# Optimization experiments

Hardware: AMD Instinct MI355X
Metric: run time of the kernel (lower is better)

The kernel has to match this reference:

```python
import jax, jax.numpy as jnp
import numpy as np

NUM_NODES = 50000
NUM_EDGES = 800000
NUM_FEATURES = 128
HIDDEN = 128
NUM_CLASSES = 40


def setup_inputs() -> dict:
    key = jax.random.key(0)
    ks = jax.random.split(key, 10)
    x = jax.random.normal(ks[0], (NUM_NODES, NUM_FEATURES), dtype=jnp.float32)
    edge_index = jax.random.randint(ks[1], (2, NUM_EDGES), 0, NUM_NODES, dtype=jnp.int32)
    def glorot(k, fan_in, fan_out):
        s = jnp.sqrt(6.0 / (fan_in + fan_out))
        return jax.random.uniform(k, (fan_in, fan_out), jnp.float32, -s, s)
    return {
        "x": x,
        "edge_index": edge_index,
        "W1": glorot(ks[2], NUM_FEATURES, HIDDEN), "b1": jnp.zeros((HIDDEN,), jnp.float32),
        "W2": glorot(ks[3], HIDDEN, HIDDEN),       "b2": jnp.zeros((HIDDEN,), jnp.float32),
        "W3": glorot(ks[4], HIDDEN, HIDDEN),       "b3": jnp.zeros((HIDDEN,), jnp.float32),
        "Wc": glorot(ks[5], HIDDEN, NUM_CLASSES),  "bc": jnp.zeros((NUM_CLASSES,), jnp.float32),
    }


def _gcn_norm(edge_index, num_nodes, dtype):
    # add self-loops, symmetric normalization D^{-1/2} (A+I) D^{-1/2}
    loops = jnp.arange(num_nodes, dtype=edge_index.dtype)
    src = jnp.concatenate([edge_index[0], loops])
    dst = jnp.concatenate([edge_index[1], loops])
    deg = jax.ops.segment_sum(jnp.ones_like(dst, dtype=dtype), dst, num_segments=num_nodes)
    dinv = jnp.where(deg > 0, jax.lax.rsqrt(deg), 0.0)
    norm = dinv[src] * dinv[dst]  # [E + N]
    return src, dst, norm


def _gcn_conv(h, W, b, src, dst, norm, num_nodes):
    h = h @ W                                  # [N, out]
    msg = h[src] * norm[:, None]               # gather + scale  [E+N, out]
    agg = jax.ops.segment_sum(msg, dst, num_segments=num_nodes)
    return agg + b


def reference(x, edge_index, W1, b1, W2, b2, W3, b3, Wc, bc):
    N = x.shape[0]
    src, dst, norm = _gcn_norm(edge_index, N, x.dtype)
    h = jax.nn.relu(_gcn_conv(x, W1, b1, src, dst, norm, N))
    h = jax.nn.relu(_gcn_conv(h, W2, b2, src, dst, norm, N))
    h = jax.nn.relu(_gcn_conv(h, W3, b3, src, dst, norm, N))
    out = h @ Wc + bc
    return (out, h)
```

## Files before the change

kernel.cpp:

```cpp
#include <hip/hip_runtime.h>

typedef float f32x4 __attribute__((ext_vector_type(4)));
typedef short s16x8 __attribute__((ext_vector_type(8)));

__device__ __forceinline__ float us2f(unsigned short u) {
    union { unsigned int i; float f; } v;
    v.i = ((unsigned int)u) << 16;
    return v.f;
}
__device__ __forceinline__ unsigned short f2us(float f) {
    union { unsigned int i; float f; } v; v.f = f;
    unsigned int r = v.i + 0x7fff + ((v.i >> 16) & 1);
    return (unsigned short)(r >> 16);
}

__global__ void k_wprep(const float* __restrict__ W1, const float* __restrict__ W2,
                        const float* __restrict__ W3, const float* __restrict__ Wc,
                        unsigned short* __restrict__ img, int* __restrict__ bcnt) {
    int b = blockIdx.x >> 7;
    int n = threadIdx.x;
    if (b >= 4) { bcnt[n] = 0; bcnt[n + 128] = 0; return; }
    int k = blockIdx.x & 127;
    unsigned short *H, *L;
    float f;
    if (b < 3) {
        const float* W = (b == 0) ? W1 : ((b == 1) ? W2 : W3);
        H = img + b * 32768; L = H + 16384;
        f = W[k * 128 + n];
    } else {
        if (n >= 48) return;
        H = img + 3 * 32768; L = H + 6144;
        f = (n < 40) ? Wc[k * 40 + n] : 0.f;
    }
    unsigned short h = f2us(f);
    unsigned short l = f2us(f - us2f(h));
    int idx = n * 128 + ((((k >> 3) ^ (n & 15))) << 3) + (k & 7);
    H[idx] = h; L[idx] = l;
}

__global__ __launch_bounds__(256) void k_hist(const int* __restrict__ dst, int E, int chunk,
                                              int* __restrict__ bcnt) {
    __shared__ int cnt[256];
    int t = threadIdx.x;
    cnt[t] = 0; __syncthreads();
    int s = blockIdx.x * chunk;
    int e = s + chunk; if (e > E) e = E;
    for (int i = s + t; i < e; i += 256) atomicAdd(&cnt[dst[i] >> 8], 1);
    __syncthreads();
    if (cnt[t]) atomicAdd(&bcnt[t], cnt[t]);
}

__global__ void k_bscan(const int* __restrict__ bcnt, int* __restrict__ bofs,
                        int* __restrict__ gcur) {
    __shared__ int s[256];
    int t = threadIdx.x;
    int v = bcnt[t];
    s[t] = v; __syncthreads();
    for (int off = 1; off < 256; off <<= 1) {
        int x = (t >= off) ? s[t - off] : 0;
        __syncthreads();
        s[t] += x;
        __syncthreads();
    }
    int ex = s[t] - v;
    bofs[t] = ex; gcur[t] = ex;
    if (t == 255) bofs[256] = s[255];
}

__global__ __launch_bounds__(256) void k_scatter1(const int* __restrict__ src,
                                                  const int* __restrict__ dst, int E, int chunk,
                                                  int* __restrict__ gcur,
                                                  unsigned int* __restrict__ pk) {
    __shared__ int cnt[256];
    int t = threadIdx.x;
    cnt[t] = 0; __syncthreads();
    int s = blockIdx.x * chunk;
    int e = s + chunk; if (e > E) e = E;
    for (int i = s + t; i < e; i += 256) atomicAdd(&cnt[dst[i] >> 8], 1);
    __syncthreads();
    int base = atomicAdd(&gcur[t], cnt[t]);
    cnt[t] = base;
    __syncthreads();
    for (int i = s + t; i < e; i += 256) {
        int d = dst[i];
        int slot = atomicAdd(&cnt[d >> 8], 1);
        pk[slot] = ((unsigned int)src[i] << 8) | (unsigned int)(d & 255);
    }
}

__global__ __launch_bounds__(256) void k_degscan(const unsigned int* __restrict__ pk,
                                                 const int* __restrict__ bofs,
                                                 int* __restrict__ row_ptr,
                                                 int* __restrict__ bsum,
                                                 float* __restrict__ dinv, int N) {
    __shared__ int cnt[256];
    __shared__ int s[256];
    int t = threadIdx.x, b = blockIdx.x;
    cnt[t] = 0; __syncthreads();
    int s0 = bofs[b], s1 = bofs[b + 1];
    for (int i = s0 + t; i < s1; i += 256) atomicAdd(&cnt[pk[i] & 255], 1);
    __syncthreads();
    int v = cnt[t];
    s[t] = v; __syncthreads();
    for (int off = 1; off < 256; off <<= 1) {
        int x = (t >= off) ? s[t - off] : 0;
        __syncthreads();
        s[t] += x;
        __syncthreads();
    }
    int node = (b << 8) + t;
    if (node < N) {
        row_ptr[node] = s[t] - v;
        dinv[node] = rsqrtf((float)(v + 1));
    }
    if (t == 255) bsum[b] = s[255];
}

__global__ void k_scan2(int* __restrict__ bsum, int nb) {
    __shared__ int s[256];
    int t = threadIdx.x;
    int v = (t < nb) ? bsum[t] : 0;
    s[t] = v; __syncthreads();
    for (int off = 1; off < 256; off <<= 1) {
        int x = (t >= off) ? s[t - off] : 0;
        __syncthreads();
        s[t] += x;
        __syncthreads();
    }
    if (t < nb) bsum[t] = s[t] - v;
}

__global__ __launch_bounds__(256) void k_scatter2(const unsigned int* __restrict__ pk,
                                                  const int* __restrict__ bofs,
                                                  int* __restrict__ row_ptr,
                                                  const int* __restrict__ bsum,
                                                  int* __restrict__ csr, int N, int E) {
    __shared__ int cur[256];
    int t = threadIdx.x, b = blockIdx.x;
    int node = (b << 8) + t;
    int rp = 0;
    if (node < N) {
        rp = row_ptr[node] + bsum[b];
        row_ptr[node] = rp;
    }
    cur[t] = rp;
    __syncthreads();
    int s = bofs[b], e = bofs[b + 1];
    for (int i = s + t; i < e; i += 256) {
        unsigned int v = pk[i];
        int slot = atomicAdd(&cur[v & 255], 1);
        csr[slot] = (int)(v >> 8);
    }
    if (node == N - 1) row_ptr[N] = E;
}

template <bool ABF16>
__global__ __launch_bounds__(256) void k_gemm128m(const void* __restrict__ Ap,
                                                  const unsigned short* __restrict__ img,
                                                  const float* __restrict__ dinv,
                                                  unsigned short* __restrict__ M, int N) {
    __shared__ __align__(16) unsigned short WsH[16384];
    __shared__ __align__(16) unsigned short WsL[16384];
    int t = threadIdx.x;
    {
        const uint4* s = (const uint4*)img;
        uint4* dH = (uint4*)WsH; uint4* dL = (uint4*)WsL;
#pragma unroll
        for (int i = 0; i < 8; i++) dH[t + i * 256] = s[t + i * 256];
#pragma unroll
        for (int i = 0; i < 8; i++) dL[t + i * 256] = s[2048 + t + i * 256];
    }
    __syncthreads();

    int w = t >> 6, lane = t & 63;
    int m = lane & 15, q = lane >> 4;
    int row0 = blockIdx.x * 64 + w * 16;
    int gr = row0 + m;
    int grc = (gr < N) ? gr : (N - 1);
    const float* A32 = (const float*)Ap + (size_t)grc * 128;
    const unsigned short* A16 = (const unsigned short*)Ap + (size_t)grc * 128;
    int nbase = m * 128;

    f32x4 acc[8];
#pragma unroll
    for (int cb = 0; cb < 8; cb++) { acc[cb][0]=0.f; acc[cb][1]=0.f; acc[cb][2]=0.f; acc[cb][3]=0.f; }

#pragma unroll
    for (int ks = 0; ks < 4; ks++) {
        union { unsigned short u[8]; s16x8 v; } ah, al;
        if constexpr (ABF16) {
            ah.v = *(const s16x8*)&A16[ks * 32 + q * 8];
        } else {
            float4 f0 = ((const float4*)A32)[ks * 8 + q * 2];
            float4 f1 = ((const float4*)A32)[ks * 8 + q * 2 + 1];
            float fv[8] = {f0.x, f0.y, f0.z, f0.w, f1.x, f1.y, f1.z, f1.w};
#pragma unroll
            for (int j = 0; j < 8; j++) {
                unsigned short h = f2us(fv[j]);
                ah.u[j] = h;
                al.u[j] = f2us(fv[j] - us2f(h));
            }
        }
        int koff = (((ks * 4 + q) ^ m) & 15) << 3;
#pragma unroll
        for (int cb = 0; cb < 8; cb++) {
            int o = cb * 2048 + nbase + koff;
            s16x8 wh = *(const s16x8*)&WsH[o];
            s16x8 wl = *(const s16x8*)&WsL[o];
            acc[cb] = __builtin_amdgcn_mfma_f32_16x16x32_bf16(ah.v, wh, acc[cb], 0, 0, 0);
            acc[cb] = __builtin_amdgcn_mfma_f32_16x16x32_bf16(ah.v, wl, acc[cb], 0, 0, 0);
            if constexpr (!ABF16)
                acc[cb] = __builtin_amdgcn_mfma_f32_16x16x32_bf16(al.v, wh, acc[cb], 0, 0, 0);
        }
    }

#pragma unroll
    for (int r = 0; r < 4; r++) {
        int grow = row0 + q * 4 + r;
        if (grow < N) {
            float dv = dinv[grow];
#pragma unroll
            for (int cb = 0; cb < 8; cb++)
                M[(size_t)grow * 128 + cb * 16 + m] = f2us(acc[cb][r] * dv);
        }
    }
}

__global__ __launch_bounds__(256) void k_gemm40m(const float* __restrict__ A,
                                                 const unsigned short* __restrict__ img,
                                                 const float* __restrict__ bc,
                                                 float* __restrict__ out, int N) {
    __shared__ __align__(16) unsigned short WsH[6144];
    __shared__ __align__(16) unsigned short WsL[6144];
    int t = threadIdx.x;
    {
        const uint4* s = (const uint4*)img;
        uint4* dH = (uint4*)WsH; uint4* dL = (uint4*)WsL;
#pragma unroll
        for (int i = 0; i < 3; i++) dH[t + i * 256] = s[t + i * 256];
#pragma unroll
        for (int i = 0; i < 3; i++) dL[t + i * 256] = s[768 + t + i * 256];
    }
    __syncthreads();

    int w = t >> 6, lane = t & 63;
    int m = lane & 15, q = lane >> 4;
    int row0 = blockIdx.x * 64 + w * 16;
    int gr = row0 + m;
    int grc = (gr < N) ? gr : (N - 1);
    const float4* Arow = (const float4*)(A + (size_t)grc * 128);
    int nbase = m * 128;

    f32x4 acc[3];
#pragma unroll
    for (int cb = 0; cb < 3; cb++) { acc[cb][0]=0.f; acc[cb][1]=0.f; acc[cb][2]=0.f; acc[cb][3]=0.f; }

#pragma unroll
    for (int ks = 0; ks < 4; ks++) {
        float4 f0 = Arow[ks * 8 + q * 2];
        float4 f1 = Arow[ks * 8 + q * 2 + 1];
        float fv[8] = {f0.x, f0.y, f0.z, f0.w, f1.x, f1.y, f1.z, f1.w};
        union { unsigned short u[8]; s16x8 v; } ah, al;
#pragma unroll
        for (int j = 0; j < 8; j++) {
            unsigned short h = f2us(fv[j]);
            ah.u[j] = h;
            al.u[j] = f2us(fv[j] - us2f(h));
        }
        int koff = (((ks * 4 + q) ^ m) & 15) << 3;
#pragma unroll
        for (int cb = 0; cb < 3; cb++) {
            int o = cb * 2048 + nbase + koff;
            s16x8 wh = *(const s16x8*)&WsH[o];
            s16x8 wl = *(const s16x8*)&WsL[o];
            acc[cb] = __builtin_amdgcn_mfma_f32_16x16x32_bf16(ah.v, wh, acc[cb], 0, 0, 0);
            acc[cb] = __builtin_amdgcn_mfma_f32_16x16x32_bf16(ah.v, wl, acc[cb], 0, 0, 0);
            acc[cb] = __builtin_amdgcn_mfma_f32_16x16x32_bf16(al.v, wh, acc[cb], 0, 0, 0);
        }
    }

#pragma unroll
    for (int r = 0; r < 4; r++) {
        int grow = row0 + q * 4 + r;
        if (grow < N) {
#pragma unroll
            for (int cb = 0; cb < 3; cb++) {
                int col = cb * 16 + m;
                if (col < 40) out[(size_t)grow * 40 + col] = acc[cb][r] + bc[col];
            }
        }
    }
}

template <bool OUT_BF16>
__global__ __launch_bounds__(256) void k_gather(const unsigned short* __restrict__ M,
                                                const int* __restrict__ csr,
                                                const int* __restrict__ row_ptr,
                                                const float* __restrict__ dinv,
                                                const float* __restrict__ bias,
                                                void* __restrict__ H, int N) {
    int w    = (blockIdx.x << 2) + (threadIdx.x >> 6);
    int lane = threadIdx.x & 63;
    if (w >= N) return;
    int g  = lane >> 4;
    int sl = lane & 15;

    const uint4* M16 = (const uint4*)M;
    float acc[8];
#pragma unroll
    for (int i = 0; i < 8; i++) acc[i] = 0.f;

    auto accum = [&](uint4 tv) {
        unsigned int uu[4] = {tv.x, tv.y, tv.z, tv.w};
#pragma unroll
        for (int i = 0; i < 4; i++) {
            acc[2 * i]     += us2f((unsigned short)(uu[i] & 0xffffu));
            acc[2 * i + 1] += us2f((unsigned short)(uu[i] >> 16));
        }
    };

    if (g == 0) accum(M16[(size_t)w * 16 + sl]);

    int s0 = row_ptr[w], s1 = row_ptr[w + 1];
    for (int base = s0; base < s1; base += 64) {
        int n = s1 - base; if (n > 64) n = 64;
        int idx = (lane < n) ? csr[base + lane] : 0;
        int full = n >> 2;
        int rem  = n & 3;
        int j = 0;
        for (; j + 4 <= full; j += 4) {
            int u0 = __shfl(idx, (j + 0) * 4 + g);
            int u1 = __shfl(idx, (j + 1) * 4 + g);
            int u2 = __shfl(idx, (j + 2) * 4 + g);
            int u3 = __shfl(idx, (j + 3) * 4 + g);
            uint4 t0 = M16[(size_t)u0 * 16 + sl];
            uint4 t1 = M16[(size_t)u1 * 16 + sl];
            uint4 t2 = M16[(size_t)u2 * 16 + sl];
            uint4 t3 = M16[(size_t)u3 * 16 + sl];
            accum(t0); accum(t1); accum(t2); accum(t3);
        }
        for (; j < full; j++) {
            int u = __shfl(idx, j * 4 + g);
            accum(M16[(size_t)u * 16 + sl]);
        }
        int ur = __shfl(idx, ((full << 2) + g) & 63);
        if (g < rem) accum(M16[(size_t)ur * 16 + sl]);
    }

#pragma unroll
    for (int i = 0; i < 8; i++) {
        acc[i] += __shfl_xor(acc[i], 16);
        acc[i] += __shfl_xor(acc[i], 32);
    }

    float dv = dinv[w];
    const float4* b4 = (const float4*)bias;
    float4 b0 = b4[sl * 2], b1 = b4[sl * 2 + 1];
    float o[8];
    o[0] = fmaxf(fmaf(dv, acc[0], b0.x), 0.f);
    o[1] = fmaxf(fmaf(dv, acc[1], b0.y), 0.f);
    o[2] = fmaxf(fmaf(dv, acc[2], b0.z), 0.f);
    o[3] = fmaxf(fmaf(dv, acc[3], b0.w), 0.f);
    o[4] = fmaxf(fmaf(dv, acc[4], b1.x), 0.f);
    o[5] = fmaxf(fmaf(dv, acc[5], b1.y), 0.f);
    o[6] = fmaxf(fmaf(dv, acc[6], b1.z), 0.f);
    o[7] = fmaxf(fmaf(dv, acc[7], b1.w), 0.f);

    if (g == 0) {
        if constexpr (OUT_BF16) {
            uint4 p;
            p.x = (unsigned int)f2us(o[0]) | ((unsigned int)f2us(o[1]) << 16);
            p.y = (unsigned int)f2us(o[2]) | ((unsigned int)f2us(o[3]) << 16);
            p.z = (unsigned int)f2us(o[4]) | ((unsigned int)f2us(o[5]) << 16);
            p.w = (unsigned int)f2us(o[6]) | ((unsigned int)f2us(o[7]) << 16);
            ((uint4*)H)[(size_t)w * 16 + sl] = p;
        } else {
            float4* H4 = (float4*)H;
            H4[(size_t)w * 32 + sl * 2]     = make_float4(o[0], o[1], o[2], o[3]);
            H4[(size_t)w * 32 + sl * 2 + 1] = make_float4(o[4], o[5], o[6], o[7]);
        }
    }
}

extern "C" void kernel_launch(void* const* d_in, const int* in_sizes, int n_in,
                              void* d_out, int out_size, void* d_ws, size_t ws_size,
                              hipStream_t stream) {
    const float* x  = (const float*)d_in[0];
    const int*   ei = (const int*)d_in[1];
    const float* W1 = (const float*)d_in[2];
    const float* b1 = (const float*)d_in[3];
    const float* W2 = (const float*)d_in[4];
    const float* b2 = (const float*)d_in[5];
    const float* W3 = (const float*)d_in[6];
    const float* b3 = (const float*)d_in[7];
    const float* Wc = (const float*)d_in[8];
    const float* bc = (const float*)d_in[9];

    const int N = in_sizes[0] / 128;
    const int E = in_sizes[1] / 2;
    const int* src = ei;
    const int* dst = ei + E;

    char* ws = (char*)d_ws;
    size_t off = 0;
    auto alloc = [&](size_t bytes) -> void* {
        void* p = ws + off;
        off = (off + bytes + 255) & ~(size_t)255;
        return p;
    };
    unsigned short* Mbuf = (unsigned short*)alloc((size_t)N * 128 * 2);
    unsigned short* Hb   = (unsigned short*)alloc((size_t)N * 128 * 2);
    unsigned int* pk     = (unsigned int*)alloc((size_t)E * 4);
    unsigned short* img  = (unsigned short*)alloc((3 * 32768 + 2 * 6144) * 2);
    float* dinv    = (float*)alloc((size_t)N * 4);
    int*   row_ptr = (int*)alloc((size_t)(N + 1) * 4);
    int*   csr     = (int*)alloc((size_t)E * 4);
    int*   bcnt    = (int*)alloc(256 * 4);
    int*   bofs    = (int*)alloc(257 * 4);
    int*   gcur    = (int*)alloc(256 * 4);
    int*   bsum    = (int*)alloc(256 * 4);

    float* out  = (float*)d_out;
    float* hbuf = out + (size_t)N * 40;

    const int nb  = (N + 255) / 256;
    const int NB  = (N + 255) >> 8;
    const int G1  = 256;
    const int chunk = (E + G1 - 1) / G1;

    k_wprep<<<513, 128, 0, stream>>>(W1, W2, W3, Wc, img, bcnt);

    k_hist<<<G1, 256, 0, stream>>>(dst, E, chunk, bcnt);
    k_bscan<<<1, 256, 0, stream>>>(bcnt, bofs, gcur);
    k_scatter1<<<G1, 256, 0, stream>>>(src, dst, E, chunk, gcur, pk);
    k_degscan<<<NB, 256, 0, stream>>>(pk, bofs, row_ptr, bsum, dinv, N);
    k_scan2<<<1, 256, 0, stream>>>(bsum, nb);
    k_scatter2<<<NB, 256, 0, stream>>>(pk, bofs, row_ptr, bsum, csr, N, E);

    const int gb  = (N + 63) / 64;
    const int gab = (N + 3) / 4;

    k_gemm128m<false><<<gb, 256, 0, stream>>>(x, img, dinv, Mbuf, N);
    k_gather<true><<<gab, 256, 0, stream>>>(Mbuf, csr, row_ptr, dinv, b1, Hb, N);
    k_gemm128m<true><<<gb, 256, 0, stream>>>(Hb, img + 32768, dinv, Mbuf, N);
    k_gather<true><<<gab, 256, 0, stream>>>(Mbuf, csr, row_ptr, dinv, b2, Hb, N);
    k_gemm128m<true><<<gb, 256, 0, stream>>>(Hb, img + 2 * 32768, dinv, Mbuf, N);
    k_gather<false><<<gab, 256, 0, stream>>>(Mbuf, csr, row_ptr, dinv, b3, hbuf, N);
    k_gemm40m<<<gb, 256, 0, stream>>>(hbuf, img + 3 * 32768, bc, out, N);
}
```

Baseline: 282.8 us.

## Fuse CSR build stages and overlap first GEMM with edge scatter

Merges weight prep with the histogram and uses a last-block-done pattern to do the bucket scan in the same kernel. The first GEMM runs in the same launch as the edge scatter. The degree scan, block-sum scan and CSR scatter become one kernel that uses an atomic counter plus a spin-wait flag as a grid barrier. To let the first GEMM run before degrees are known, the source-side dinv scaling moves from the GEMM epilogue into the gather. This adds a per-neighbor dinv load in every aggregation. The aim is fewer kernel launches and less serialization, but the spin-wait relies on all blocks being co-resident.

After: 288.1 us. No clear change (+1.9%).

```diff
diff --git a/kernel.cpp b/kernel.cpp
--- a/kernel.cpp
+++ b/kernel.cpp
@@ -14,154 +14,68 @@
     return (unsigned short)(r >> 16);
 }
 
-__global__ void k_wprep(const float* __restrict__ W1, const float* __restrict__ W2,
-                        const float* __restrict__ W3, const float* __restrict__ Wc,
-                        unsigned short* __restrict__ img, int* __restrict__ bcnt) {
-    int b = blockIdx.x >> 7;
-    int n = threadIdx.x;
-    if (b >= 4) { bcnt[n] = 0; bcnt[n + 128] = 0; return; }
-    int k = blockIdx.x & 127;
-    unsigned short *H, *L;
-    float f;
-    if (b < 3) {
-        const float* W = (b == 0) ? W1 : ((b == 1) ? W2 : W3);
-        H = img + b * 32768; L = H + 16384;
-        f = W[k * 128 + n];
-    } else {
-        if (n >= 48) return;
-        H = img + 3 * 32768; L = H + 6144;
-        f = (n < 40) ? Wc[k * 40 + n] : 0.f;
-    }
-    unsigned short h = f2us(f);
-    unsigned short l = f2us(f - us2f(h));
-    int idx = n * 128 + ((((k >> 3) ^ (n & 15))) << 3) + (k & 7);
-    H[idx] = h; L[idx] = l;
-}
-
-__global__ __launch_bounds__(256) void k_hist(const int* __restrict__ dst, int E, int chunk,
-                                              int* __restrict__ bcnt) {
+__global__ __launch_bounds__(256) void k_prep_hist(const float* __restrict__ W1,
+                                                   const float* __restrict__ W2,
+                                                   const float* __restrict__ W3,
+                                                   const float* __restrict__ Wc,
+                                                   unsigned short* __restrict__ img,
+                                                   const int* __restrict__ dst, int E, int chunk,
+                                                   int* __restrict__ bcnt, int* __restrict__ done,
+                                                   int* __restrict__ bofs, int* __restrict__ gcur) {
     __shared__ int cnt[256];
+    __shared__ int lastflag;
     int t = threadIdx.x;
+    if (blockIdx.x < 256) {
+        int r = (blockIdx.x << 1) | (t >> 7);
+        int b = r >> 7, k = r & 127, n = t & 127;
+        unsigned short *H, *L;
+        float f;
+        if (b < 3) {
+            const float* W = (b == 0) ? W1 : ((b == 1) ? W2 : W3);
+            H = img + b * 32768; L = H + 16384;
+            f = W[k * 128 + n];
+        } else {
+            if (n >= 48) return;
+            H = img + 3 * 32768; L = H + 6144;
+            f = (n < 40) ? Wc[k * 40 + n] : 0.f;
+        }
+        unsigned short h = f2us(f);
+        unsigned short l = f2us(f - us2f(h));
+        int idx = n * 128 + ((((k >> 3) ^ (n & 15))) << 3) + (k & 7);
+        H[idx] = h; L[idx] = l;
+        return;
+    }
     cnt[t] = 0; __syncthreads();
-    int s = blockIdx.x * chunk;
-    int e = s + chunk; if (e > E) e = E;
-    for (int i = s + t; i < e; i += 256) atomicAdd(&cnt[dst[i] >> 8], 1);
-    __syncthreads();
-    if (cnt[t]) atomicAdd(&bcnt[t], cnt[t]);
-}
-
-__global__ void k_bscan(const int* __restrict__ bcnt, int* __restrict__ bofs,
-                        int* __restrict__ gcur) {
-    __shared__ int s[256];
-    int t = threadIdx.x;
-    int v = bcnt[t];
-    s[t] = v; __syncthreads();
+    int blk = blockIdx.x - 256;
+    int s0 = blk * chunk;
+    int s1 = s0 + chunk; if (s1 > E) s1 = E;
+    for (int i = s0 + t; i < s1; i += 256) atomicAdd(&cnt[dst[i] >> 8], 1);
+    __syncthreads();
+    int c = cnt[t];
+    if (c) atomicAdd(&bcnt[t], c);
+    __syncthreads();
+    if (t == 0) { __threadfence(); lastflag = (atomicAdd(done, 1) == 255); }
+    __syncthreads();
+    if (!lastflag) return;
+    int v = __hip_atomic_load(&bcnt[t], __ATOMIC_RELAXED, __HIP_MEMORY_SCOPE_AGENT);
+    cnt[t] = v; __syncthreads();
     for (int off = 1; off < 256; off <<= 1) {
-        int x = (t >= off) ? s[t - off] : 0;
-        __syncthreads();
-        s[t] += x;
-        __syncthreads();
-    }
-    int ex = s[t] - v;
+        int x = (t >= off) ? cnt[t - off] : 0;
+        __syncthreads();
+        cnt[t] += x;
+        __syncthreads();
+    }
+    int ex = cnt[t] - v;
     bofs[t] = ex; gcur[t] = ex;
-    if (t == 255) bofs[256] = s[255];
-}
-
-__global__ __launch_bounds__(256) void k_scatter1(const int* __restrict__ src,
-                                                  const int* __restrict__ dst, int E, int chunk,
-                                                  int* __restrict__ gcur,
-                                                  unsigned int* __restrict__ pk) {
-    __shared__ int cnt[256];
-    int t = threadIdx.x;
-    cnt[t] = 0; __syncthreads();
-    int s = blockIdx.x * chunk;
-    int e = s + chunk; if (e > E) e = E;
-    for (int i = s + t; i < e; i += 256) atomicAdd(&cnt[dst[i] >> 8], 1);
-    __syncthreads();
-    int base = atomicAdd(&gcur[t], cnt[t]);
-    cnt[t] = base;
-    __syncthreads();
-    for (int i = s + t; i < e; i += 256) {
-        int d = dst[i];
-        int slot = atomicAdd(&cnt[d >> 8], 1);
-        pk[slot] = ((unsigned int)src[i] << 8) | (unsigned int)(d & 255);
-    }
-}
-
-__global__ __launch_bounds__(256) void k_degscan(const unsigned int* __restrict__ pk,
-                                                 const int* __restrict__ bofs,
-                                                 int* __restrict__ row_ptr,
-                                                 int* __restrict__ bsum,
-                                                 float* __restrict__ dinv, int N) {
-    __shared__ int cnt[256];
-    __shared__ int s[256];
-    int t = threadIdx.x, b = blockIdx.x;
-    cnt[t] = 0; __syncthreads();
-    int s0 = bofs[b], s1 = bofs[b + 1];
-    for (int i = s0 + t; i < s1; i += 256) atomicAdd(&cnt[pk[i] & 255], 1);
-    __syncthreads();
-    int v = cnt[t];
-    s[t] = v; __syncthreads();
-    for (int off = 1; off < 256; off <<= 1) {
-        int x = (t >= off) ? s[t - off] : 0;
-        __syncthreads();
-        s[t] += x;
-        __syncthreads();
-    }
-    int node = (b << 8) + t;
-    if (node < N) {
-        row_ptr[node] = s[t] - v;
-        dinv[node] = rsqrtf((float)(v + 1));
-    }
-    if (t == 255) bsum[b] = s[255];
-}
-
-__global__ void k_scan2(int* __restrict__ bsum, int nb) {
-    __shared__ int s[256];
-    int t = threadIdx.x;
-    int v = (t < nb) ? bsum[t] : 0;
-    s[t] = v; __syncthreads();
-    for (int off = 1; off < 256; off <<= 1) {
-        int x = (t >= off) ? s[t - off] : 0;
-        __syncthreads();
-        s[t] += x;
-        __syncthreads();
-    }
-    if (t < nb) bsum[t] = s[t] - v;
-}
-
-__global__ __launch_bounds__(256) void k_scatter2(const unsigned int* __restrict__ pk,
-                                                  const int* __restrict__ bofs,
-                                                  int* __restrict__ row_ptr,
-                                                  const int* __restrict__ bsum,
-                                                  int* __restrict__ csr, int N, int E) {
-    __shared__ int cur[256];
-    int t = threadIdx.x, b = blockIdx.x;
-    int node = (b << 8) + t;
-    int rp = 0;
-    if (node < N) {
-        rp = row_ptr[node] + bsum[b];
-        row_ptr[node] = rp;
-    }
-    cur[t] = rp;
-    __syncthreads();
-    int s = bofs[b], e = bofs[b + 1];
-    for (int i = s + t; i < e; i += 256) {
-        unsigned int v = pk[i];
-        int slot = atomicAdd(&cur[v & 255], 1);
-        csr[slot] = (int)(v >> 8);
-    }
-    if (node == N - 1) row_ptr[N] = E;
+    if (t == 255) bofs[256] = cnt[255];
 }
 
 template <bool ABF16>
-__global__ __launch_bounds__(256) void k_gemm128m(const void* __restrict__ Ap,
-                                                  const unsigned short* __restrict__ img,
-                                                  const float* __restrict__ dinv,
-                                                  unsigned short* __restrict__ M, int N) {
-    __shared__ __align__(16) unsigned short WsH[16384];
-    __shared__ __align__(16) unsigned short WsL[16384];
-    int t = threadIdx.x;
+__device__ __forceinline__ void gemm128_core(const void* __restrict__ Ap,
+                                             const unsigned short* __restrict__ img,
+                                             unsigned short* __restrict__ M, int N,
+                                             int bid, int t,
+                                             unsigned short* WsH, unsigned short* WsL) {
     {
         const uint4* s = (const uint4*)img;
         uint4* dH = (uint4*)WsH; uint4* dL = (uint4*)WsL;
@@ -174,7 +88,7 @@
 
     int w = t >> 6, lane = t & 63;
     int m = lane & 15, q = lane >> 4;
-    int row0 = blockIdx.x * 64 + w * 16;
+    int row0 = bid * 64 + w * 16;
     int gr = row0 + m;
     int grc = (gr < N) ? gr : (N - 1);
     const float* A32 = (const float*)Ap + (size_t)grc * 128;
@@ -218,78 +132,115 @@
     for (int r = 0; r < 4; r++) {
         int grow = row0 + q * 4 + r;
         if (grow < N) {
-            float dv = dinv[grow];
 #pragma unroll
             for (int cb = 0; cb < 8; cb++)
-                M[(size_t)grow * 128 + cb * 16 + m] = f2us(acc[cb][r] * dv);
-        }
-    }
-}
-
-__global__ __launch_bounds__(256) void k_gemm40m(const float* __restrict__ A,
-                                                 const unsigned short* __restrict__ img,
-                                                 const float* __restrict__ bc,
-                                                 float* __restrict__ out, int N) {
-    __shared__ __align__(16) unsigned short WsH[6144];
-    __shared__ __align__(16) unsigned short WsL[6144];
+                M[(size_t)grow * 128 + cb * 16 + m] = f2us(acc[cb][r]);
+        }
+    }
+}
+
+template <bool ABF16>
+__global__ __launch_bounds__(256) void k_gemm128m(const void* __restrict__ Ap,
+                                                  const unsigned short* __restrict__ img,
+                                                  unsigned short* __restrict__ M, int N) {
+    __shared__ __align__(16) unsigned short WsH[16384];
+    __shared__ __align__(16) unsigned short WsL[16384];
+    gemm128_core<ABF16>(Ap, img, M, N, blockIdx.x, threadIdx.x, WsH, WsL);
+}
+
+union KSM {
+    struct { unsigned short H[16384]; unsigned short L[16384]; } w;
+    int cnt[256];
+};
+__global__ __launch_bounds__(256) void k_sc1_gemm1(const int* __restrict__ src,
+                                                   const int* __restrict__ dst, int E, int chunk,
+                                                   int* __restrict__ gcur,
+                                                   unsigned int* __restrict__ pk,
+                                                   const float* __restrict__ x,
+                                                   const unsigned short* __restrict__ img,
+                                                   unsigned short* __restrict__ M, int N) {
+    __shared__ __align__(16) KSM sm;
     int t = threadIdx.x;
-    {
-        const uint4* s = (const uint4*)img;
-        uint4* dH = (uint4*)WsH; uint4* dL = (uint4*)WsL;
-#pragma unroll
-        for (int i = 0; i < 3; i++) dH[t + i * 256] = s[t + i * 256];
-#pragma unroll
-        for (int i = 0; i < 3; i++) dL[t + i * 256] = s[768 + t + i * 256];
-    }
-    __syncthreads();
-
-    int w = t >> 6, lane = t & 63;
-    int m = lane & 15, q = lane >> 4;
-    int row0 = blockIdx.x * 64 + w * 16;
-    int gr = row0 + m;
-    int grc = (gr < N) ? gr : (N - 1);
-    const float4* Arow = (const float4*)(A + (size_t)grc * 128);
-    int nbase = m * 128;
-
-    f32x4 acc[3];
-#pragma unroll
-    for (int cb = 0; cb < 3; cb++) { acc[cb][0]=0.f; acc[cb][1]=0.f; acc[cb][2]=0.f; acc[cb][3]=0.f; }
-
-#pragma unroll
-    for (int ks = 0; ks < 4; ks++) {
-        float4 f0 = Arow[ks * 8 + q * 2];
-        float4 f1 = Arow[ks * 8 + q * 2 + 1];
-        float fv[8] = {f0.x, f0.y, f0.z, f0.w, f1.x, f1.y, f1.z, f1.w};
-        union { unsigned short u[8]; s16x8 v; } ah, al;
-#pragma unroll
-        for (int j = 0; j < 8; j++) {
-            unsigned short h = f2us(fv[j]);
-            ah.u[j] = h;
-            al.u[j] = f2us(fv[j] - us2f(h));
-        }
-        int koff = (((ks * 4 + q) ^ m) & 15) << 3;
-#pragma unroll
-        for (int cb = 0; cb < 3; cb++) {
-            int o = cb * 2048 + nbase + koff;
-            s16x8 wh = *(const s16x8*)&WsH[o];
-            s16x8 wl = *(const s16x8*)&WsL[o];
-            acc[cb] = __builtin_amdgcn_mfma_f32_16x16x32_bf16(ah.v, wh, acc[cb], 0, 0, 0);
-            acc[cb] = __builtin_amdgcn_mfma_f32_16x16x32_bf16(ah.v, wl, acc[cb], 0, 0, 0);
-            acc[cb] = __builtin_amdgcn_mfma_f32_16x16x32_bf16(al.v, wh, acc[cb], 0, 0, 0);
-        }
-    }
-
-#pragma unroll
-    for (int r = 0; r < 4; r++) {
-        int grow = row0 + q * 4 + r;
-        if (grow < N) {
-#pragma unroll
-            for (int cb = 0; cb < 3; cb++) {
-                int col = cb * 16 + m;
-                if (col < 40) out[(size_t)grow * 40 + col] = acc[cb][r] + bc[col];
-            }
-        }
-    }
+    if (blockIdx.x < 256) {
+        sm.cnt[t] = 0; __syncthreads();
+        int s0 = blockIdx.x * chunk;
+        int s1 = s0 + chunk; if (s1 > E) s1 = E;
+        for (int i = s0 + t; i < s1; i += 256) atomicAdd(&sm.cnt[dst[i] >> 8], 1);
+        __syncthreads();
+        int base = atomicAdd(&gcur[t], sm.cnt[t]);
+        sm.cnt[t] = base;
+        __syncthreads();
+        for (int i = s0 + t; i < s1; i += 256) {
+            int d = dst[i];
+            int slot = atomicAdd(&sm.cnt[d >> 8], 1);
+            pk[slot] = ((unsigned int)src[i] << 8) | (unsigned int)(d & 255);
+        }
+        return;
+    }
+    gemm128_core<false>(x, img, M, N, blockIdx.x - 256, t, sm.w.H, sm.w.L);
+}
+
+__global__ __launch_bounds__(256) void k_csr_finish(const unsigned int* __restrict__ pk,
+                                                    const int* __restrict__ bofs,
+                                                    int* __restrict__ row_ptr,
+                                                    int* __restrict__ bsum,
+                                                    float* __restrict__ dinv,
+                                                    int* __restrict__ csr,
+                                                    int N, int E, int nb,
+                                                    int* __restrict__ done2,
+                                                    int* __restrict__ flag3) {
+    __shared__ int cnt[256];
+    __shared__ int s[256];
+    __shared__ int lastflag;
+    int t = threadIdx.x, b = blockIdx.x;
+    cnt[t] = 0; __syncthreads();
+    int s0 = bofs[b], s1 = bofs[b + 1];
+    for (int i = s0 + t; i < s1; i += 256) atomicAdd(&cnt[pk[i] & 255], 1);
+    __syncthreads();
+    int v = cnt[t];
+    s[t] = v; __syncthreads();
+    for (int off = 1; off < 256; off <<= 1) {
+        int x = (t >= off) ? s[t - off] : 0;
+        __syncthreads();
+        s[t] += x;
+        __syncthreads();
+    }
+    int node = (b << 8) + t;
+    int rp_local = s[t] - v;
+    if (node < N) dinv[node] = rsqrtf((float)(v + 1));
+    if (t == 255) __hip_atomic_store(&bsum[b], s[255], __ATOMIC_RELAXED, __HIP_MEMORY_SCOPE_AGENT);
+    __syncthreads();
+    if (t == 0) { __threadfence(); lastflag = (atomicAdd(done2, 1) == nb - 1); }
+    __syncthreads();
+    if (lastflag) {
+        int vv = (t < nb) ? __hip_atomic_load(&bsum[t], __ATOMIC_RELAXED, __HIP_MEMORY_SCOPE_AGENT) : 0;
+        s[t] = vv; __syncthreads();
+        for (int off = 1; off < 256; off <<= 1) {
+            int x = (t >= off) ? s[t - off] : 0;
+            __syncthreads();
+            s[t] += x;
+            __syncthreads();
+        }
+        if (t < nb) __hip_atomic_store(&bsum[t], s[t] - vv, __ATOMIC_RELAXED, __HIP_MEMORY_SCOPE_AGENT);
+        __syncthreads();
+        if (t == 0) { __threadfence(); __hip_atomic_store(flag3, 1, __ATOMIC_RELEASE, __HIP_MEMORY_SCOPE_AGENT); }
+    }
+    if (t == 0) {
+        while (__hip_atomic_load(flag3, __ATOMIC_ACQUIRE, __HIP_MEMORY_SCOPE_AGENT) == 0)
+            __builtin_amdgcn_s_sleep(2);
+    }
+    __syncthreads();
+    int base = __hip_atomic_load(&bsum[b], __ATOMIC_RELAXED, __HIP_MEMORY_SCOPE_AGENT);
+    int rp = 0;
+    if (node < N) { rp = rp_local + base; row_ptr[node] = rp; }
+    cnt[t] = rp;
+    __syncthreads();
+    for (int i = s0 + t; i < s1; i += 256) {
+        unsigned int vpk = pk[i];
+        int slot = atomicAdd(&cnt[vpk & 255], 1);
+        csr[slot] = (int)(vpk >> 8);
+    }
+    if (node == N - 1) row_ptr[N] = E;
 }
 
 template <bool OUT_BF16>
@@ -306,20 +257,21 @@
     int sl = lane & 15;
 
     const uint4* M16 = (const uint4*)M;
+    float dv = dinv[w];
     float acc[8];
 #pragma unroll
     for (int i = 0; i < 8; i++) acc[i] = 0.f;
 
-    auto accum = [&](uint4 tv) {
+    auto accum = [&](uint4 tv, float sc) {
         unsigned int uu[4] = {tv.x, tv.y, tv.z, tv.w};
 #pragma unroll
         for (int i = 0; i < 4; i++) {
-            acc[2 * i]     += us2f((unsigned short)(uu[i] & 0xffffu));
-            acc[2 * i + 1] += us2f((unsigned short)(uu[i] >> 16));
+            acc[2 * i]     = fmaf(sc, us2f((unsigned short)(uu[i] & 0xffffu)), acc[2 * i]);
+            acc[2 * i + 1] = fmaf(sc, us2f((unsigned short)(uu[i] >> 16)), acc[2 * i + 1]);
         }
     };
 
-    if (g == 0) accum(M16[(size_t)w * 16 + sl]);
+    if (g == 0) accum(M16[(size_t)w * 16 + sl], dv);
 
     int s0 = row_ptr[w], s1 = row_ptr[w + 1];
     for (int base = s0; base < s1; base += 64) {
@@ -333,18 +285,19 @@
             int u1 = __shfl(idx, (j + 1) * 4 + g);
             int u2 = __shfl(idx, (j + 2) * 4 + g);
             int u3 = __shfl(idx, (j + 3) * 4 + g);
+            float d0 = dinv[u0], d1 = dinv[u1], d2 = dinv[u2], d3 = dinv[u3];
             uint4 t0 = M16[(size_t)u0 * 16 + sl];
             uint4 t1 = M16[(size_t)u1 * 16 + sl];
             uint4 t2 = M16[(size_t)u2 * 16 + sl];
             uint4 t3 = M16[(size_t)u3 * 16 + sl];
-            accum(t0); accum(t1); accum(t2); accum(t3);
+            accum(t0, d0); accum(t1, d1); accum(t2, d2); accum(t3, d3);
         }
         for (; j < full; j++) {
             int u = __shfl(idx, j * 4 + g);
-            accum(M16[(size_t)u * 16 + sl]);
+            accum(M16[(size_t)u * 16 + sl], dinv[u]);
         }
         int ur = __shfl(idx, ((full << 2) + g) & 63);
-        if (g < rem) accum(M16[(size_t)ur * 16 + sl]);
+        if (g < rem) accum(M16[(size_t)ur * 16 + sl], dinv[ur]);
     }
 
 #pragma unroll
@@ -353,7 +306,6 @@
         acc[i] += __shfl_xor(acc[i], 32);
     }
 
-    float dv = dinv[w];
     const float4* b4 = (const float4*)bias;
     float4 b0 = b4[sl * 2], b1 = b4[sl * 2 + 1];
     float o[8];
@@ -378,6 +330,72 @@
             float4* H4 = (float4*)H;
             H4[(size_t)w * 32 + sl * 2]     = make_float4(o[0], o[1], o[2], o[3]);
             H4[(size_t)w * 32 + sl * 2 + 1] = make_float4(o[4], o[5], o[6], o[7]);
+        }
+    }
+}
+
+__global__ __launch_bounds__(256) void k_gemm40m(const float* __restrict__ A,
+                                                 const unsigned short* __restrict__ img,
+                                                 const float* __restrict__ bc,
+                                                 float* __restrict__ out, int N) {
+    __shared__ __align__(16) unsigned short WsH[6144];
+    __shared__ __align__(16) unsigned short WsL[6144];
+    int t = threadIdx.x;
+    {
+        const uint4* s = (const uint4*)img;
+        uint4* dH = (uint4*)WsH; uint4* dL = (uint4*)WsL;
+#pragma unroll
+        for (int i = 0; i < 3; i++) dH[t + i * 256] = s[t + i * 256];
+#pragma unroll
+        for (int i = 0; i < 3; i++) dL[t + i * 256] = s[768 + t + i * 256];
+    }
+    __syncthreads();
+
+    int w = t >> 6, lane = t & 63;
+    int m = lane & 15, q = lane >> 4;
+    int row0 = blockIdx.x * 64 + w * 16;
+    int gr = row0 + m;
+    int grc = (gr < N) ? gr : (N - 1);
+    const float4* Arow = (const float4*)(A + (size_t)grc * 128);
+    int nbase = m * 128;
+
+    f32x4 acc[3];
+#pragma unroll
+    for (int cb = 0; cb < 3; cb++) { acc[cb][0]=0.f; acc[cb][1]=0.f; acc[cb][2]=0.f; acc[cb][3]=0.f; }
+
+#pragma unroll
+    for (int ks = 0; ks < 4; ks++) {
+        float4 f0 = Arow[ks * 8 + q * 2];
+        float4 f1 = Arow[ks * 8 + q * 2 + 1];
+        float fv[8] = {f0.x, f0.y, f0.z, f0.w, f1.x, f1.y, f1.z, f1.w};
+        union { unsigned short u[8]; s16x8 v; } ah, al;
+#pragma unroll
+        for (int j = 0; j < 8; j++) {
+            unsigned short h = f2us(fv[j]);
+            ah.u[j] = h;
+            al.u[j] = f2us(fv[j] - us2f(h));
+        }
+        int koff = (((ks * 4 + q) ^ m) & 15) << 3;
+#pragma unroll
+        for (int cb = 0; cb < 3; cb++) {
+            int o = cb * 2048 + nbase + koff;
+            s16x8 wh = *(const s16x8*)&WsH[o];
+            s16x8 wl = *(const s16x8*)&WsL[o];
+            acc[cb] = __builtin_amdgcn_mfma_f32_16x16x32_bf16(ah.v, wh, acc[cb], 0, 0, 0);
+            acc[cb] = __builtin_amdgcn_mfma_f32_16x16x32_bf16(ah.v, wl, acc[cb], 0, 0, 0);
+            acc[cb] = __builtin_amdgcn_mfma_f32_16x16x32_bf16(al.v, wh, acc[cb], 0, 0, 0);
+        }
+    }
+
+#pragma unroll
+    for (int r = 0; r < 4; r++) {
+        int grow = row0 + q * 4 + r;
+        if (grow < N) {
+#pragma unroll
+            for (int cb = 0; cb < 3; cb++) {
+                int col = cb * 16 + m;
+                if (col < 40) out[(size_t)grow * 40 + col] = acc[cb][r] + bc[col];
+            }
         }
     }
 }
@@ -415,36 +433,38 @@
     float* dinv    = (float*)alloc((size_t)N * 4);
     int*   row_ptr = (int*)alloc((size_t)(N + 1) * 4);
     int*   csr     = (int*)alloc((size_t)E * 4);
-    int*   bcnt    = (int*)alloc(256 * 4);
+    int*   ctrl    = (int*)alloc(512 * 4);
     int*   bofs    = (int*)alloc(257 * 4);
     int*   gcur    = (int*)alloc(256 * 4);
     int*   bsum    = (int*)alloc(256 * 4);
 
+    int* bcnt  = ctrl;
+    int* done  = ctrl + 256;
+    int* done2 = ctrl + 257;
+    int* flag3 = ctrl + 258;
+
     float* out  = (float*)d_out;
     float* hbuf = out + (size_t)N * 40;
 
     const int nb  = (N + 255) / 256;
-    const int NB  = (N + 255) >> 8;
-    const int G1  = 256;
-    const int chunk = (E + G1 - 1) / G1;
-
-    k_wprep<<<513, 128, 0, stream>>>(W1, W2, W3, Wc, img, bcnt);
-
-    k_hist<<<G1, 256, 0, stream>>>(dst, E, chunk, bcnt);
-    k_bscan<<<1, 256, 0, stream>>>(bcnt, bofs, gcur);
-    k_scatter1<<<G1, 256, 0, stream>>>(src, dst, E, chunk, gcur, pk);
-    k_degscan<<<NB, 256, 0, stream>>>(pk, bofs, row_ptr, bsum, dinv, N);
-    k_scan2<<<1, 256, 0, stream>>>(bsum, nb);
-    k_scatter2<<<NB, 256, 0, stream>>>(pk, bofs, row_ptr, bsum, csr, N, E);
+    const int chunk = (E + 255) / 256;
 
     const int gb  = (N + 63) / 64;
     const int gab = (N + 3) / 4;
 
-    k_gemm128m<false><<<gb, 256, 0, stream>>>(x, img, dinv, Mbuf, N);
+    hipMemsetAsync(ctrl, 0, 512 * 4, stream);
+
+    k_prep_hist<<<512, 256, 0, stream>>>(W1, W2, W3, Wc, img, dst, E, chunk,
+                                         bcnt, done, bofs, gcur);
+    k_sc1_gemm1<<<256 + gb, 256, 0, stream>>>(src, dst, E, chunk, gcur, pk,
+                                              x, img, Mbuf, N);
+    k_csr_finish<<<nb, 256, 0, stream>>>(pk, bofs, row_ptr, bsum, dinv, csr,
+                                         N, E, nb, done2, flag3);
+
     k_gather<true><<<gab, 256, 0, stream>>>(Mbuf, csr, row_ptr, dinv, b1, Hb, N);
-    k_gemm128m<true><<<gb, 256, 0, stream>>>(Hb, img + 32768, dinv, Mbuf, N);
+    k_gemm128m<true><<<gb, 256, 0, stream>>>(Hb, img + 32768, Mbuf, N);
     k_gather<true><<<gab, 256, 0, stream>>>(Mbuf, csr, row_ptr, dinv, b2, Hb, N);
-    k_gemm128m<true><<<gb, 256, 0, stream>>>(Hb, img + 2 * 32768, dinv, Mbuf, N);
+    k_gemm128m<true><<<gb, 256, 0, stream>>>(Hb, img + 2 * 32768, Mbuf, N);
     k_gather<false><<<gab, 256, 0, stream>>>(Mbuf, csr, row_ptr, dinv, b3, hbuf, N);
     k_gemm40m<<<gb, 256, 0, stream>>>(hbuf, img + 3 * 32768, bc, out, N);
 }
```
